# Kernel tuning notes

Hardware: AMD Instinct MI355X
Metric: run time of the kernel (lower is better)

The kernel has to match this reference:

```python
import jax, jax.numpy as jnp
import numpy as np

PHI = 3.1415926 * 0.3   # Cosine_fMRI default phi (data_dim=-1 -> A=1)
MIN_NORM = 1e-15
PROJ_EPS = 4e-3         # float32 eps used by hyperbolic project


def _project(x, c):
    # Clip to the Poincare ball of curvature c (norm over last dim).
    norm = jnp.maximum(jnp.linalg.norm(x, axis=-1, keepdims=True), MIN_NORM)
    maxnorm = (1.0 - PROJ_EPS) / jnp.sqrt(c)
    return jnp.where(norm > maxnorm, x / norm * maxnorm, x)


def _logmap0(x, c):
    sqrt_c = jnp.sqrt(c)
    norm = jnp.maximum(jnp.linalg.norm(x, axis=-1, keepdims=True), MIN_NORM)
    arg = jnp.clip(sqrt_c * norm, -1.0 + MIN_NORM, 1.0 - MIN_NORM)
    return jnp.arctanh(arg) / (sqrt_c * norm) * x


def _fkernel(x, c):
    return _logmap0(_project(x, c), c)


def _act(x, a):
    # F.relu(x) + a * cos(x + phi)  (Cosine_fMRI with A=1)
    return jax.nn.relu(x) + a * jnp.cos(x + PHI)


def _corr_abs(data):
    # data: [B, T, N]; per-sample |corrcoef| between ROIs -> [B, N, N]
    xm = data - jnp.mean(data, axis=1, keepdims=True)
    cov = jnp.einsum('btn,btm->bnm', xm, xm)
    d = jnp.sqrt(jnp.diagonal(cov, axis1=-2, axis2=-1))  # [B, N]
    corr = cov / (d[:, :, None] * d[:, None, :])
    return jnp.abs(jnp.nan_to_num(corr))


def _normalize_adj(adj):
    # D^-1/2 (A+I) D^-1/2 per block (block-diag structure -> batched dense)
    B, N, _ = adj.shape
    A = adj + jnp.eye(N, dtype=adj.dtype)
    dinv = jnp.power(jnp.sum(A, axis=-1), -0.5)  # [B, N]
    return dinv[:, :, None] * A * dinv[:, None, :]


def setup_inputs() -> dict:
    key = jax.random.key(0)
    ks = jax.random.split(key, 3)
    B, T, N, H = 256, 240, 264, 256
    data = jax.random.normal(ks[0], (B, T, N), dtype=jnp.float32)
    # kaiming_uniform-style init for GCN weights
    b1w = np.sqrt(6.0 / N)
    b2w = np.sqrt(6.0 / H)
    W1 = jax.random.uniform(ks[1], (N, H), jnp.float32, -b1w, b1w)
    W2 = jax.random.uniform(ks[2], (H, H), jnp.float32, -b2w, b2w)
    b1 = jnp.zeros((H,), jnp.float32)
    b2 = jnp.zeros((H,), jnp.float32)
    return {"data": data, "W1": W1, "b1": b1, "W2": W2, "b2": b2}


def reference(data, W1, b1, W2, b2):
    c = jnp.float32(1.0)
    a = jnp.float32(0.5)  # a_fMRI
    adj = _corr_abs(data)          # [B, N, N]; also the input features
    L = _normalize_adj(adj)        # [B, N, N]
    # GCN layer 1: L @ (fea @ W1) + b1  (batched == block-diag sparse.mm)
    x1 = jnp.einsum('bij,bjh->bih', L, adj @ W1) + b1
    g1 = _act(_fkernel(x1, c), a)
    x2 = jnp.einsum('bij,bjh->bih', L, g1 @ W2) + b2
    g2 = _act(_fkernel(x2, c), a)  # [B, N, H]
    return g2, adj
```

## Files before the change

kernel.cpp:

```cpp
#include <hip/hip_runtime.h>
#include <hip/hip_bf16.h>
#include <math.h>

#define B_ 256
#define T_ 240
#define N_ 264
#define H_ 256
#define BN_ (B_ * N_)
#define PHI_ 0.94247778f
#define MAXNORM_ 0.996f

typedef short short8 __attribute__((ext_vector_type(8)));
typedef float f32x4 __attribute__((ext_vector_type(4)));
typedef unsigned short ushort4v __attribute__((ext_vector_type(4)));

__device__ inline unsigned short f2bf(float f) {
  __hip_bfloat16 h = __float2bfloat16(f);
  return *reinterpret_cast<unsigned short*>(&h);
}
__device__ inline float bf2f(unsigned short u) {
  unsigned int x = ((unsigned int)u) << 16;
  return __uint_as_float(x);
}

__device__ inline int swz16(int row, int kg) {
  return row * 4 + ((kg ^ (row >> 1)) & 3);
}

__device__ inline void gload_lds16(const void* g, void* l) {
  __builtin_amdgcn_global_load_lds(
      (const __attribute__((address_space(1))) unsigned int*)g,
      (__attribute__((address_space(3))) unsigned int*)l, 16, 0, 0);
}

__global__ __launch_bounds__(256) void zTs_kernel(
    const float* __restrict__ data, unsigned short* __restrict__ z) {
  int b = blockIdx.y;
  int n0 = blockIdx.x * 64;
  __shared__ float ld[240 * 65];
  __shared__ float ps[4][64], pq[4][64];
  __shared__ float mS[64], rS[64];
  int tid = threadIdx.x, lane = tid & 63, wv = tid >> 6;
  int n = n0 + lane;
  bool nv = n < N_;
  for (int t = wv; t < T_; t += 4)
    ld[t * 65 + lane] = nv ? data[((size_t)b * T_ + t) * N_ + n] : 0.f;
  __syncthreads();
  {
    int col = tid & 63, q = tid >> 6;
    float s = 0.f, ss = 0.f;
    for (int t = q * 60; t < q * 60 + 60; ++t) { float v = ld[t * 65 + col]; s += v; ss += v * v; }
    ps[q][col] = s; pq[q][col] = ss;
  }
  __syncthreads();
  if (tid < 64) {
    float s  = ps[0][tid] + ps[1][tid] + ps[2][tid] + ps[3][tid];
    float ss = pq[0][tid] + pq[1][tid] + pq[2][tid] + pq[3][tid];
    float m = s / (float)T_;
    float var = ss - s * m;
    float d = sqrtf(fmaxf(var, 0.f));
    mS[tid] = m;
    rS[tid] = (d > 0.f) ? (1.f / d) : 0.f;
  }
  __syncthreads();
  int nrows = min(64, N_ - n0);
  for (int rr = 0; rr < nrows; ++rr) {
    float m = mS[rr], r = rS[rr];
    unsigned short val = (tid < T_) ? f2bf((ld[tid * 65 + rr] - m) * r) : (unsigned short)0;
    z[((size_t)(b * N_ + n0 + rr)) * 256 + tid] = val;
  }
}

__global__ __launch_bounds__(256) void wtrans_kernel(
    const float* __restrict__ W, unsigned short* __restrict__ WT,
    int Jv, int Jpad) {
  int jt = blockIdx.x * 64, ht = blockIdx.y * 64;
  __shared__ float tile[64][65];
  int tid = threadIdx.x;
  for (int idx = tid; idx < 4096; idx += 256) {
    int jr = idx >> 6, hr = idx & 63;
    int j = jt + jr;
    tile[jr][hr] = (j < Jv) ? W[(size_t)j * H_ + ht + hr] : 0.f;
  }
  __syncthreads();
  for (int idx = tid; idx < 4096; idx += 256) {
    int hr = idx >> 6, jr = idx & 63;
    int j = jt + jr;
    if (j < Jpad) WT[(size_t)(ht + hr) * Jpad + j] = f2bf(tile[jr][hr]);
  }
}

template<int EPI>
__global__ __launch_bounds__(256) void mfma_gemm_kernel(
    const unsigned short* __restrict__ A, int lda, long sA, int rowsA,
    const unsigned short* __restrict__ Bm, int ldb, long sB, int validB,
    int ksteps,
    float* __restrict__ outF, unsigned short* __restrict__ outB,
    float* __restrict__ dsum, const float* __restrict__ bias) {
  int gx = gridDim.x, gy = gridDim.y;
  int flat = (blockIdx.z * gy + blockIdx.y) * gx + blockIdx.x;
  int nwg = gx * gy * gridDim.z;
  int q8 = nwg >> 3;
  int id = (flat & 7) * q8 + (flat >> 3);
  int bx = id % gx; int tq = id / gx;
  int b = tq / gy;
  int i0 = (tq % gy) * 64;
  int n0 = bx * 256;

  int tid = threadIdx.x;
  int w = tid >> 6, lane = tid & 63, g = lane >> 4, l4 = lane & 15;

  __shared__ short8 AsV[2][256];
  __shared__ short8 BsV[2][1024];

  const unsigned short* Ab = A + (size_t)b * sA;
  const unsigned short* Bb = Bm + (size_t)b * sB;

  f32x4 acc[4][4];
#pragma unroll
  for (int x = 0; x < 4; ++x)
#pragma unroll
    for (int y = 0; y < 4; ++y) acc[x][y] = (f32x4){0.f, 0.f, 0.f, 0.f};

  const unsigned short* aSrc;
  {
    int s = w * 64 + lane;
    int row = s >> 2, kg = (s & 3) ^ ((s >> 3) & 3);
    int rA = min(i0 + row, rowsA - 1);
    aSrc = Ab + (size_t)rA * lda + kg * 8;
  }
  const unsigned short* bSrc[4];
#pragma unroll
  for (int c = 0; c < 4; ++c) {
    int s = w * 256 + c * 64 + lane;
    int col = s >> 2, kg = (s & 3) ^ ((s >> 3) & 3);
    bSrc[c] = Bb + (size_t)(n0 + col) * ldb + kg * 8;
  }
  bool wactive = (n0 + w * 64) < validB;

  gload_lds16(aSrc, &AsV[0][w * 64]);
#pragma unroll
  for (int c = 0; c < 4; ++c) gload_lds16(bSrc[c], &BsV[0][w * 256 + c * 64]);
  __syncthreads();

  int cur = 0;
  for (int ks = 0; ks < ksteps; ++ks) {
    if (ks + 1 < ksteps) {
      int k1 = (ks + 1) * 32;
      gload_lds16(aSrc + k1, &AsV[cur ^ 1][w * 64]);
#pragma unroll
      for (int c = 0; c < 4; ++c) gload_lds16(bSrc[c] + k1, &BsV[cur ^ 1][w * 256 + c * 64]);
    }
    if (wactive) {
      short8 af[4], bfr[4];
#pragma unroll
      for (int fr = 0; fr < 4; ++fr) af[fr] = AsV[cur][swz16(fr * 16 + l4, g)];
#pragma unroll
      for (int fc = 0; fc < 4; ++fc) bfr[fc] = BsV[cur][swz16(w * 64 + fc * 16 + l4, g)];
#pragma unroll
      for (int fr = 0; fr < 4; ++fr)
#pragma unroll
        for (int fc = 0; fc < 4; ++fc)
          acc[fr][fc] = __builtin_amdgcn_mfma_f32_16x16x32_bf16(af[fr], bfr[fc], acc[fr][fc], 0, 0, 0);
    }
    __syncthreads();
    cur ^= 1;
  }

  if constexpr (EPI == 0) {
    __shared__ float rsum[64][4];
#pragma unroll
    for (int fr = 0; fr < 4; ++fr) {
      int rb = i0 + fr * 16 + g * 4;
      float sr[4] = {0.f, 0.f, 0.f, 0.f};
#pragma unroll
      for (int fc = 0; fc < 4; ++fc) {
        int j = n0 + w * 64 + fc * 16 + l4;
#pragma unroll
        for (int reg = 0; reg < 4; ++reg) {
          int i = rb + reg;
          float v = fabsf(acc[fr][fc][reg]);
          if (i < N_ && j < N_) outF[((size_t)b * N_ + i) * N_ + j] = v;
          if (i < N_ && j < 288) outB[((size_t)b * N_ + i) * 288 + j] = f2bf(j < N_ ? v : 0.f);
          if (j < N_) sr[reg] += v;
        }
      }
#pragma unroll
      for (int reg = 0; reg < 4; ++reg) {
        float s = sr[reg];
        s += __shfl_xor(s, 1); s += __shfl_xor(s, 2);
        s += __shfl_xor(s, 4); s += __shfl_xor(s, 8);
        if (l4 == 0) rsum[fr * 16 + g * 4 + reg][w] = s;
      }
    }
    __syncthreads();
    if (tid < 64) {
      int i = i0 + tid;
      if (i < N_)
        atomicAdd(&dsum[(size_t)b * N_ + i],
                  rsum[tid][0] + rsum[tid][1] + rsum[tid][2] + rsum[tid][3]);
    }
  }

  if constexpr (EPI == 1) {
#pragma unroll
    for (int fr = 0; fr < 4; ++fr) {
      int rb = i0 + fr * 16 + g * 4;
      if (rb < 288) {
        float dv[4];
#pragma unroll
        for (int reg = 0; reg < 4; ++reg) {
          int j = rb + reg;
          dv[reg] = (j < N_) ? (1.f / sqrtf(1.f + dsum[(size_t)b * N_ + j])) : 0.f;
        }
#pragma unroll
        for (int fc = 0; fc < 4; ++fc) {
          int col = w * 64 + fc * 16 + l4;
          ushort4v pk;
#pragma unroll
          for (int reg = 0; reg < 4; ++reg)
            pk[reg] = f2bf(dv[reg] * acc[fr][fc][reg]);
          *(ushort4v*)(outB + ((size_t)b * H_ + col) * 288 + rb) = pk;
        }
      }
    }
  }

  if constexpr (EPI >= 2) {
    __shared__ float rs[64][4];
    float ratio[4][4];
#pragma unroll
    for (int fr = 0; fr < 4; ++fr) {
      int rb = i0 + fr * 16 + g * 4;
      int rbc = min(rb, 284);
      float din[4];
#pragma unroll
      for (int reg = 0; reg < 4; ++reg) {
        int ic = min(rb + reg, N_ - 1);
        din[reg] = 1.f / sqrtf(1.f + dsum[(size_t)b * N_ + ic]);
      }
#pragma unroll
      for (int fc = 0; fc < 4; ++fc) {
        int col = w * 64 + fc * 16 + l4;
        ushort4v dy = *(const ushort4v*)(Bb + (size_t)col * ldb + rbc);
        float bias_v = bias[col];
#pragma unroll
        for (int reg = 0; reg < 4; ++reg) {
          float x = din[reg] * (acc[fr][fc][reg] + bf2f(dy[reg])) + bias_v;
          acc[fr][fc][reg] = x;
        }
      }
    }
#pragma unroll
    for (int fr = 0; fr < 4; ++fr) {
#pragma unroll
      for (int reg = 0; reg < 4; ++reg) {
        float s = 0.f;
#pragma unroll
        for (int fc = 0; fc < 4; ++fc) { float x = acc[fr][fc][reg]; s += x * x; }
        s += __shfl_xor(s, 1); s += __shfl_xor(s, 2);
        s += __shfl_xor(s, 4); s += __shfl_xor(s, 8);
        if (l4 == 0) rs[fr * 16 + g * 4 + reg][w] = s;
      }
    }
    __syncthreads();
#pragma unroll
    for (int fr = 0; fr < 4; ++fr)
#pragma unroll
      for (int reg = 0; reg < 4; ++reg) {
        int r = fr * 16 + g * 4 + reg;
        float tot = rs[r][0] + rs[r][1] + rs[r][2] + rs[r][3];
        float norm = fmaxf(sqrtf(tot), 1e-15f);
        float scale = (norm > MAXNORM_) ? (MAXNORM_ / norm) : 1.0f;
        float pn = fmaxf(fminf(norm, MAXNORM_), 1e-15f);
        ratio[fr][reg] = atanhf(pn) / pn * scale;
      }
#pragma unroll
    for (int fr = 0; fr < 4; ++fr) {
      int rb = i0 + fr * 16 + g * 4;
#pragma unroll
      for (int fc = 0; fc < 4; ++fc) {
        int col = w * 64 + fc * 16 + l4;
#pragma unroll
        for (int reg = 0; reg < 4; ++reg) {
          int row = rb + reg;
          if (row < N_) {
            float y = ratio[fr][reg] * acc[fr][fc][reg];
            float o = fmaxf(y, 0.f) + 0.5f * __cosf(y + PHI_);
            if constexpr (EPI == 2) outB[((size_t)b * N_ + row) * H_ + col] = f2bf(o);
            else                    outF[((size_t)b * N_ + row) * H_ + col] = o;
          }
        }
      }
    }
  }
}

extern "C" void kernel_launch(void* const* d_in, const int* in_sizes, int n_in,
                              void* d_out, int out_size, void* d_ws, size_t ws_size,
                              hipStream_t stream) {
  const float* data = (const float*)d_in[0];
  const float* W1   = (const float*)d_in[1];
  const float* b1   = (const float*)d_in[2];
  const float* W2   = (const float*)d_in[3];
  const float* b2   = (const float*)d_in[4];

  float* g2   = (float*)d_out;
  float* adjF = g2 + (size_t)B_ * N_ * H_;

  float* ws_f = (float*)d_ws;
  float* dsum = ws_f;
  unsigned short* region1 = (unsigned short*)(ws_f + BN_);
  unsigned short* z    = region1;
  unsigned short* YT   = region1;
  unsigned short* W1T  = region1 + (size_t)B_ * H_ * 288;
  unsigned short* W2T  = W1T + (size_t)H_ * 288;
  unsigned short* adjB = W2T + (size_t)H_ * H_;
  unsigned short* g1bf = (unsigned short*)d_out;

  hipMemsetAsync(dsum, 0, BN_ * sizeof(float), stream);
  zTs_kernel<<<dim3(5, B_), 256, 0, stream>>>(data, z);
  wtrans_kernel<<<dim3(5, 4), 256, 0, stream>>>(W1, W1T, N_, 288);
  wtrans_kernel<<<dim3(4, 4), 256, 0, stream>>>(W2, W2T, H_, 256);
  mfma_gemm_kernel<0><<<dim3(2, 5, B_), 256, 0, stream>>>(
      z, 256, (long)N_ * 256, N_, z, 256, (long)N_ * 256, N_, 8,
      adjF, adjB, dsum, nullptr);
  mfma_gemm_kernel<1><<<dim3(1, 5, B_), 256, 0, stream>>>(
      adjB, 288, (long)N_ * 288, N_, W1T, 288, 0L, 256, 9,
      nullptr, YT, dsum, nullptr);
  mfma_gemm_kernel<2><<<dim3(1, 5, B_), 256, 0, stream>>>(
      adjB, 288, (long)N_ * 288, N_, YT, 288, (long)H_ * 288, 256, 9,
      nullptr, g1bf, dsum, b1);
  mfma_gemm_kernel<1><<<dim3(1, 5, B_), 256, 0, stream>>>(
      g1bf, 256, (long)N_ * 256, N_, W2T, 256, 0L, 256, 8,
      nullptr, YT, dsum, nullptr);
  mfma_gemm_kernel<3><<<dim3(1, 5, B_), 256, 0, stream>>>(
      adjB, 288, (long)N_ * 288, N_, YT, 288, (long)H_ * 288, 256, 9,
      g2, nullptr, dsum, b2);
}
```

Baseline: 602.2 us.

## Split z normalization into stats pass and tiled transpose, skip inactive B loads

Replaces the single zTs kernel, which staged a 240x65 float tile in LDS per block, with two kernels. The first computes per-ROI mean and inverse std with one thread per column. The second transposes 64x64 tiles through a small LDS buffer and writes packed 4-element bf16 stores. The aim is to cut the old kernel's large LDS footprint so more blocks fit per CU, and to replace its 2-byte scalar stores with vector stores. In exchange the input data is read twice and there is one extra launch. The GEMM also skips B-tile loads for waves that do no MFMA work, saving some memory traffic on edge tiles.

```diff
diff --git a/kernel.cpp b/kernel.cpp
--- a/kernel.cpp
+++ b/kernel.cpp
@@ -33,41 +33,63 @@
       (__attribute__((address_space(3))) unsigned int*)l, 16, 0, 0);
 }
 
-__global__ __launch_bounds__(256) void zTs_kernel(
-    const float* __restrict__ data, unsigned short* __restrict__ z) {
-  int b = blockIdx.y;
-  int n0 = blockIdx.x * 64;
-  __shared__ float ld[240 * 65];
-  __shared__ float ps[4][64], pq[4][64];
+__global__ __launch_bounds__(512) void stats2_kernel(
+    const float* __restrict__ data, float* __restrict__ mean, float* __restrict__ rd) {
+  int b = blockIdx.x;
+  int n = threadIdx.x;
+  if (n >= N_) return;
+  const float* db = data + (size_t)b * T_ * N_ + n;
+  float s = 0.f, ss = 0.f;
+#pragma unroll 8
+  for (int t = 0; t < T_; ++t) {
+    float v = db[(size_t)t * N_];
+    s += v; ss += v * v;
+  }
+  float m = s / (float)T_;
+  float var = ss - s * m;
+  float d = sqrtf(fmaxf(var, 0.f));
+  mean[b * N_ + n] = m;
+  rd[b * N_ + n] = (d > 0.f) ? (1.f / d) : 0.f;
+}
+
+__global__ __launch_bounds__(256) void ztile_kernel(
+    const float* __restrict__ data, const float* __restrict__ mean,
+    const float* __restrict__ rd, unsigned short* __restrict__ z) {
+  int b = blockIdx.y, n0 = blockIdx.x * 64;
+  __shared__ float tile[64][65];
   __shared__ float mS[64], rS[64];
-  int tid = threadIdx.x, lane = tid & 63, wv = tid >> 6;
-  int n = n0 + lane;
-  bool nv = n < N_;
-  for (int t = wv; t < T_; t += 4)
-    ld[t * 65 + lane] = nv ? data[((size_t)b * T_ + t) * N_ + n] : 0.f;
-  __syncthreads();
-  {
-    int col = tid & 63, q = tid >> 6;
-    float s = 0.f, ss = 0.f;
-    for (int t = q * 60; t < q * 60 + 60; ++t) { float v = ld[t * 65 + col]; s += v; ss += v * v; }
-    ps[q][col] = s; pq[q][col] = ss;
-  }
-  __syncthreads();
+  int tid = threadIdx.x;
   if (tid < 64) {
-    float s  = ps[0][tid] + ps[1][tid] + ps[2][tid] + ps[3][tid];
-    float ss = pq[0][tid] + pq[1][tid] + pq[2][tid] + pq[3][tid];
-    float m = s / (float)T_;
-    float var = ss - s * m;
-    float d = sqrtf(fmaxf(var, 0.f));
-    mS[tid] = m;
-    rS[tid] = (d > 0.f) ? (1.f / d) : 0.f;
-  }
-  __syncthreads();
-  int nrows = min(64, N_ - n0);
-  for (int rr = 0; rr < nrows; ++rr) {
-    float m = mS[rr], r = rS[rr];
-    unsigned short val = (tid < T_) ? f2bf((ld[tid * 65 + rr] - m) * r) : (unsigned short)0;
-    z[((size_t)(b * N_ + n0 + rr)) * 256 + tid] = val;
+    int n = n0 + tid;
+    mS[tid] = (n < N_) ? mean[b * N_ + n] : 0.f;
+    rS[tid] = (n < N_) ? rd[b * N_ + n] : 0.f;
+  }
+  const float* db = data + (size_t)b * T_ * N_;
+  int e = tid & 15, rbase = tid >> 4;
+  for (int sub = 0; sub < 4; ++sub) {
+    int t0 = sub * 64;
+    __syncthreads();
+    for (int idx = tid; idx < 4096; idx += 256) {
+      int tl = idx >> 6, nl = idx & 63;
+      int t = t0 + tl, n = n0 + nl;
+      tile[tl][nl] = (t < T_ && n < N_) ? db[(size_t)t * N_ + n] : 0.f;
+    }
+    __syncthreads();
+#pragma unroll
+    for (int i = 0; i < 4; ++i) {
+      int r = rbase + 16 * i;
+      int n_r = n0 + r;
+      if (n_r < N_) {
+        float m = mS[r], rr_ = rS[r];
+        ushort4v pk;
+#pragma unroll
+        for (int j = 0; j < 4; ++j) {
+          int tl = e * 4 + j;
+          pk[j] = (t0 + tl < T_) ? f2bf((tile[tl][r] - m) * rr_) : (unsigned short)0;
+        }
+        *(ushort4v*)(z + ((size_t)(b * N_ + n_r)) * 256 + t0 + e * 4) = pk;
+      }
+    }
   }
 }
 
@@ -139,8 +161,10 @@
   bool wactive = (n0 + w * 64) < validB;
 
   gload_lds16(aSrc, &AsV[0][w * 64]);
-#pragma unroll
-  for (int c = 0; c < 4; ++c) gload_lds16(bSrc[c], &BsV[0][w * 256 + c * 64]);
+  if (wactive) {
+#pragma unroll
+    for (int c = 0; c < 4; ++c) gload_lds16(bSrc[c], &BsV[0][w * 256 + c * 64]);
+  }
   __syncthreads();
 
   int cur = 0;
@@ -148,8 +172,10 @@
     if (ks + 1 < ksteps) {
       int k1 = (ks + 1) * 32;
       gload_lds16(aSrc + k1, &AsV[cur ^ 1][w * 64]);
-#pragma unroll
-      for (int c = 0; c < 4; ++c) gload_lds16(bSrc[c] + k1, &BsV[cur ^ 1][w * 256 + c * 64]);
+      if (wactive) {
+#pragma unroll
+        for (int c = 0; c < 4; ++c) gload_lds16(bSrc[c] + k1, &BsV[cur ^ 1][w * 256 + c * 64]);
+      }
     }
     if (wactive) {
       short8 af[4], bfr[4];
@@ -310,7 +336,9 @@
 
   float* ws_f = (float*)d_ws;
   float* dsum = ws_f;
-  unsigned short* region1 = (unsigned short*)(ws_f + BN_);
+  float* mean = ws_f + BN_;
+  float* rd   = ws_f + 2 * BN_;
+  unsigned short* region1 = (unsigned short*)(ws_f + 3 * BN_);
   unsigned short* z    = region1;
   unsigned short* YT   = region1;
   unsigned short* W1T  = region1 + (size_t)B_ * H_ * 288;
@@ -319,7 +347,8 @@
   unsigned short* g1bf = (unsigned short*)d_out;
 
   hipMemsetAsync(dsum, 0, BN_ * sizeof(float), stream);
-  zTs_kernel<<<dim3(5, B_), 256, 0, stream>>>(data, z);
+  stats2_kernel<<<B_, 512, 0, stream>>>(data, mean, rd);
+  ztile_kernel<<<dim3(5, B_), 256, 0, stream>>>(data, mean, rd, z);
   wtrans_kernel<<<dim3(5, 4), 256, 0, stream>>>(W1, W1T, N_, 288);
   wtrans_kernel<<<dim3(4, 4), 256, 0, stream>>>(W2, W2T, H_, 256);
   mfma_gemm_kernel<0><<<dim3(2, 5, B_), 256, 0, stream>>>(
```

Result: faster. 554.8 us (-7.9%).
